# Performance work log

Measured on AMD Instinct MI355X. Metric: run time of the kernel, lower is better.

Reference implementation:

```python
import jax, jax.numpy as jnp
import numpy as np

INPUT_DIM = 64
HIDDEN_DIM = 128
N_ROWS = 2_000_000
N_GROUPS = 2


def setup_inputs() -> dict:
    key = jax.random.key(0)
    k_x, k_T, k_w1, k_b1, k_w2, k_b2 = jax.random.split(key, 6)
    x = jax.random.normal(k_x, (N_ROWS, INPUT_DIM), dtype=jnp.float32)
    T = jax.random.randint(k_T, (N_ROWS,), 0, N_GROUPS, dtype=jnp.int64)
    # Linear params (torch convention: W @ x layout -> y = x @ W.T + b)
    lim1 = 1.0 / np.sqrt(INPUT_DIM)
    W1 = jax.random.uniform(k_w1, (HIDDEN_DIM, INPUT_DIM), jnp.float32, -lim1, lim1)
    b1 = jax.random.uniform(k_b1, (HIDDEN_DIM,), jnp.float32, -lim1, lim1)
    lim2 = 1.0 / np.sqrt(HIDDEN_DIM)
    W2 = jax.random.uniform(k_w2, (1, HIDDEN_DIM), jnp.float32, -lim2, lim2)
    b2 = jax.random.uniform(k_b2, (1,), jnp.float32, -lim2, lim2)
    return {"x": x, "T": T, "W1": W1, "b1": b1, "W2": W2, "b2": b2}


def reference(x, T, W1, b1, W2, b2):
    # s = f2(tanh(f1(x))).flatten()  -> [N]
    h = jnp.tanh(x @ W1.T + b1)                      # [N, H]
    s = (h @ W2.T + b2).reshape(-1)                  # [N]
    e = jnp.exp(s)                                   # faithful to torch.exp (unshifted)
    # group sums via segment_sum (2 groups), then gather-normalize per row
    sums = jax.ops.segment_sum(e, T, num_segments=N_GROUPS)  # [2]
    return e / sums[T]
```

## Files before the change

### kernel.cpp

```cpp
#include <hip/hip_runtime.h>
#include <math.h>

#define NROWS 2000000
#define IN_DIM 64
#define HID 128
#define NTILES (NROWS / 16)

typedef __bf16 bf16x8 __attribute__((ext_vector_type(8)));
typedef float f32x4 __attribute__((ext_vector_type(4)));

__device__ __forceinline__ float tanh_fast(float a) {
    float p = __expf(2.0f * a);
    float r = __builtin_amdgcn_rcpf(p + 1.0f);
    return fmaf(-2.0f, r, 1.0f);
}

__device__ __forceinline__ void split8(f32x4 a, f32x4 b, bf16x8& h, bf16x8& l) {
    #pragma unroll
    for (int j = 0; j < 4; j++) {
        __bf16 hb = (__bf16)a[j];
        h[j] = hb;
        l[j] = (__bf16)(a[j] - (float)hb);
    }
    #pragma unroll
    for (int j = 0; j < 4; j++) {
        __bf16 hb = (__bf16)b[j];
        h[4 + j] = hb;
        l[4 + j] = (__bf16)(b[j] - (float)hb);
    }
}

__global__ void zero_sums_kernel(float* g) {
    if (threadIdx.x < 2) g[threadIdx.x] = 0.0f;
}

__global__ __launch_bounds__(256, 2) void fused_mfma_kernel(
    const float* __restrict__ x, const int* __restrict__ T,
    const float* __restrict__ W1, const float* __restrict__ b1,
    const float* __restrict__ W2, const float* __restrict__ b2,
    float* __restrict__ e_out, float* __restrict__ gsums)
{
    const int lane = threadIdx.x & 63;
    const int c16  = lane & 15;
    const int g4   = lane >> 4;
    const int gwave = blockIdx.x * (blockDim.x >> 6) + (threadIdx.x >> 6);
    const int nwave = gridDim.x * (blockDim.x >> 6);

    int tile = gwave;
    f32x4 xq0, xq1, xq2, xq3;
    {
        const float* xp = x + (size_t)(tile * 16 + c16) * IN_DIM + g4 * 8;
        xq0 = *(const f32x4*)(xp);
        xq1 = *(const f32x4*)(xp + 4);
        xq2 = *(const f32x4*)(xp + 32);
        xq3 = *(const f32x4*)(xp + 36);
    }

    bf16x8 w1h[8][2], w1l[8][2];
    #pragma unroll
    for (int t = 0; t < 8; t++) {
        #pragma unroll
        for (int c = 0; c < 2; c++) {
            const float* wp = W1 + (size_t)(t * 16 + c16) * IN_DIM + c * 32 + g4 * 8;
            f32x4 a = *(const f32x4*)wp;
            f32x4 b = *(const f32x4*)(wp + 4);
            split8(a, b, w1h[t][c], w1l[t][c]);
        }
    }
    float b1v[8], w2v[8];
    #pragma unroll
    for (int t = 0; t < 8; t++) {
        b1v[t] = b1[t * 16 + c16];
        w2v[t] = W2[t * 16 + c16];
    }
    const float b2v = b2[0];

    float ls0 = 0.f, ls1 = 0.f;

    for (; tile < NTILES; tile += nwave) {
        bf16x8 xh0, xh1, xl0, xl1;
        split8(xq0, xq1, xh0, xl0);
        split8(xq2, xq3, xh1, xl1);

        int nt = tile + nwave;
        if (nt < NTILES) {
            const float* xp = x + (size_t)(nt * 16 + c16) * IN_DIM + g4 * 8;
            xq0 = *(const f32x4*)(xp);
            xq1 = *(const f32x4*)(xp + 4);
            xq2 = *(const f32x4*)(xp + 32);
            xq3 = *(const f32x4*)(xp + 36);
        }

        f32x4 acc[8];
        #pragma unroll
        for (int t = 0; t < 8; t++) acc[t] = (f32x4){0.f, 0.f, 0.f, 0.f};
        #pragma unroll
        for (int t = 0; t < 8; t++) {
            acc[t] = __builtin_amdgcn_mfma_f32_16x16x32_bf16(xh0, w1h[t][0], acc[t], 0, 0, 0);
            acc[t] = __builtin_amdgcn_mfma_f32_16x16x32_bf16(xl0, w1h[t][0], acc[t], 0, 0, 0);
            acc[t] = __builtin_amdgcn_mfma_f32_16x16x32_bf16(xh0, w1l[t][0], acc[t], 0, 0, 0);
            acc[t] = __builtin_amdgcn_mfma_f32_16x16x32_bf16(xl0, w1l[t][0], acc[t], 0, 0, 0);
            acc[t] = __builtin_amdgcn_mfma_f32_16x16x32_bf16(xh1, w1h[t][1], acc[t], 0, 0, 0);
            acc[t] = __builtin_amdgcn_mfma_f32_16x16x32_bf16(xl1, w1h[t][1], acc[t], 0, 0, 0);
            acc[t] = __builtin_amdgcn_mfma_f32_16x16x32_bf16(xh1, w1l[t][1], acc[t], 0, 0, 0);
            acc[t] = __builtin_amdgcn_mfma_f32_16x16x32_bf16(xl1, w1l[t][1], acc[t], 0, 0, 0);
        }

        float sp0 = 0.f, sp1 = 0.f, sp2 = 0.f, sp3 = 0.f;
        #pragma unroll
        for (int t = 0; t < 8; t++) {
            sp0 = fmaf(tanh_fast(acc[t][0] + b1v[t]), w2v[t], sp0);
            sp1 = fmaf(tanh_fast(acc[t][1] + b1v[t]), w2v[t], sp1);
            sp2 = fmaf(tanh_fast(acc[t][2] + b1v[t]), w2v[t], sp2);
            sp3 = fmaf(tanh_fast(acc[t][3] + b1v[t]), w2v[t], sp3);
        }
        #pragma unroll
        for (int m = 1; m < 16; m <<= 1) {
            sp0 += __shfl_xor(sp0, m, 16);
            sp1 += __shfl_xor(sp1, m, 16);
            sp2 += __shfl_xor(sp2, m, 16);
            sp3 += __shfl_xor(sp3, m, 16);
        }
        if (c16 < 4) {
            float sv = (c16 == 0) ? sp0 : (c16 == 1) ? sp1 : (c16 == 2) ? sp2 : sp3;
            float e = __expf(sv + b2v);
            int row = tile * 16 + g4 * 4 + c16;
            e_out[row] = e;
            if (T[row] == 0) ls0 += e; else ls1 += e;
        }
    }

    #pragma unroll
    for (int off = 32; off > 0; off >>= 1) {
        ls0 += __shfl_down(ls0, off, 64);
        ls1 += __shfl_down(ls1, off, 64);
    }
    if (lane == 0) {
        atomicAdd(&gsums[0], ls0);
        atomicAdd(&gsums[1], ls1);
    }
}

__global__ __launch_bounds__(256) void normalize_kernel(
    float* __restrict__ e_out, const int* __restrict__ T,
    const float* __restrict__ gsums)
{
    const float inv0 = 1.0f / gsums[0];
    const float inv1 = 1.0f / gsums[1];
    const int n4 = NROWS / 4;
    const int stride = gridDim.x * blockDim.x;
    for (int i = blockIdx.x * blockDim.x + threadIdx.x; i < n4; i += stride) {
        float4 e = reinterpret_cast<const float4*>(e_out)[i];
        int4  t = reinterpret_cast<const int4*>(T)[i];
        e.x *= (t.x == 0) ? inv0 : inv1;
        e.y *= (t.y == 0) ? inv0 : inv1;
        e.z *= (t.z == 0) ? inv0 : inv1;
        e.w *= (t.w == 0) ? inv0 : inv1;
        reinterpret_cast<float4*>(e_out)[i] = e;
    }
}

extern "C" void kernel_launch(void* const* d_in, const int* in_sizes, int n_in,
                              void* d_out, int out_size, void* d_ws, size_t ws_size,
                              hipStream_t stream) {
    const float* x  = (const float*)d_in[0];
    const int*   T  = (const int*)d_in[1];
    const float* W1 = (const float*)d_in[2];
    const float* b1 = (const float*)d_in[3];
    const float* W2 = (const float*)d_in[4];
    const float* b2 = (const float*)d_in[5];
    float* e_out = (float*)d_out;
    float* gsums = (float*)d_ws;

    zero_sums_kernel<<<1, 64, 0, stream>>>(gsums);

    fused_mfma_kernel<<<512, 256, 0, stream>>>(x, T, W1, b1, W2, b2, e_out, gsums);

    normalize_kernel<<<2048, 256, 0, stream>>>(e_out, T, gsums);
}
```

Before: 199.1 us.

## Switch to single fp16 MFMA pass with LDS-staged weights and DPP reductions

```diff
diff --git a/kernel.cpp b/kernel.cpp
--- a/kernel.cpp
+++ b/kernel.cpp
@@ -5,8 +5,11 @@
 #define IN_DIM 64
 #define HID 128
 #define NTILES (NROWS / 16)
+#define BLOCK 256
+#define NBLK 1024
+#define WPB (BLOCK / 64)
 
-typedef __bf16 bf16x8 __attribute__((ext_vector_type(8)));
+typedef _Float16 half8 __attribute__((ext_vector_type(8)));
 typedef float f32x4 __attribute__((ext_vector_type(4)));
 
 __device__ __forceinline__ float tanh_fast(float a) {
@@ -15,58 +18,52 @@
     return fmaf(-2.0f, r, 1.0f);
 }
 
-__device__ __forceinline__ void split8(f32x4 a, f32x4 b, bf16x8& h, bf16x8& l) {
-    #pragma unroll
-    for (int j = 0; j < 4; j++) {
-        __bf16 hb = (__bf16)a[j];
-        h[j] = hb;
-        l[j] = (__bf16)(a[j] - (float)hb);
-    }
-    #pragma unroll
-    for (int j = 0; j < 4; j++) {
-        __bf16 hb = (__bf16)b[j];
-        h[4 + j] = hb;
-        l[4 + j] = (__bf16)(b[j] - (float)hb);
-    }
+__device__ __forceinline__ float dpp_row_sum16(float v) {
+    int x;
+    x = __float_as_int(v);
+    v += __int_as_float(__builtin_amdgcn_update_dpp(0, x, 0x111, 0xf, 0xf, true));
+    x = __float_as_int(v);
+    v += __int_as_float(__builtin_amdgcn_update_dpp(0, x, 0x112, 0xf, 0xf, true));
+    x = __float_as_int(v);
+    v += __int_as_float(__builtin_amdgcn_update_dpp(0, x, 0x114, 0xf, 0xf, true));
+    x = __float_as_int(v);
+    v += __int_as_float(__builtin_amdgcn_update_dpp(0, x, 0x118, 0xf, 0xf, true));
+    return v;
 }
 
 __global__ void zero_sums_kernel(float* g) {
     if (threadIdx.x < 2) g[threadIdx.x] = 0.0f;
 }
 
-__global__ __launch_bounds__(256, 2) void fused_mfma_kernel(
+__global__ __launch_bounds__(BLOCK, 4) void fused_mfma_kernel(
     const float* __restrict__ x, const int* __restrict__ T,
     const float* __restrict__ W1, const float* __restrict__ b1,
     const float* __restrict__ W2, const float* __restrict__ b2,
     float* __restrict__ e_out, float* __restrict__ gsums)
 {
+    __shared__ _Float16 wlds[8][2][64][8];
+
     const int lane = threadIdx.x & 63;
+    const int wv   = threadIdx.x >> 6;
     const int c16  = lane & 15;
     const int g4   = lane >> 4;
-    const int gwave = blockIdx.x * (blockDim.x >> 6) + (threadIdx.x >> 6);
-    const int nwave = gridDim.x * (blockDim.x >> 6);
 
-    int tile = gwave;
-    f32x4 xq0, xq1, xq2, xq3;
-    {
-        const float* xp = x + (size_t)(tile * 16 + c16) * IN_DIM + g4 * 8;
-        xq0 = *(const f32x4*)(xp);
-        xq1 = *(const f32x4*)(xp + 4);
-        xq2 = *(const f32x4*)(xp + 32);
-        xq3 = *(const f32x4*)(xp + 36);
-    }
-
-    bf16x8 w1h[8][2], w1l[8][2];
     #pragma unroll
-    for (int t = 0; t < 8; t++) {
+    for (int tt = 0; tt < 2; tt++) {
+        const int t = wv * 2 + tt;
+        const int n = t * 16 + c16;
         #pragma unroll
         for (int c = 0; c < 2; c++) {
-            const float* wp = W1 + (size_t)(t * 16 + c16) * IN_DIM + c * 32 + g4 * 8;
-            f32x4 a = *(const f32x4*)wp;
-            f32x4 b = *(const f32x4*)(wp + 4);
-            split8(a, b, w1h[t][c], w1l[t][c]);
+            const int kb = c * 32 + g4 * 8;
+            half8 h;
+            #pragma unroll
+            for (int j = 0; j < 8; j++)
+                h[j] = (_Float16)W1[n * IN_DIM + kb + j];
+            *(half8*)&wlds[t][c][lane][0] = h;
         }
     }
+    __syncthreads();
+
     float b1v[8], w2v[8];
     #pragma unroll
     for (int t = 0; t < 8; t++) {
@@ -75,20 +72,38 @@
     }
     const float b2v = b2[0];
 
+    const int gwave = blockIdx.x * WPB + wv;
+    const int nwave = NBLK * WPB;
+
     float ls0 = 0.f, ls1 = 0.f;
 
+    int tile = gwave;
+    f32x4 g0, g1, g2, g3;
+    {
+        const float* xp = x + (size_t)tile * 1024 + (size_t)c16 * IN_DIM + g4 * 8;
+        g0 = *(const f32x4*)(xp);
+        g1 = *(const f32x4*)(xp + 4);
+        g2 = *(const f32x4*)(xp + 32);
+        g3 = *(const f32x4*)(xp + 36);
+    }
+
     for (; tile < NTILES; tile += nwave) {
-        bf16x8 xh0, xh1, xl0, xl1;
-        split8(xq0, xq1, xh0, xl0);
-        split8(xq2, xq3, xh1, xl1);
+        half8 xf0, xf1;
+        #pragma unroll
+        for (int j = 0; j < 4; j++) {
+            xf0[j]     = (_Float16)g0[j];
+            xf0[4 + j] = (_Float16)g1[j];
+            xf1[j]     = (_Float16)g2[j];
+            xf1[4 + j] = (_Float16)g3[j];
+        }
 
-        int nt = tile + nwave;
+        const int nt = tile + nwave;
         if (nt < NTILES) {
-            const float* xp = x + (size_t)(nt * 16 + c16) * IN_DIM + g4 * 8;
-            xq0 = *(const f32x4*)(xp);
-            xq1 = *(const f32x4*)(xp + 4);
-            xq2 = *(const f32x4*)(xp + 32);
-            xq3 = *(const f32x4*)(xp + 36);
+            const float* xp = x + (size_t)nt * 1024 + (size_t)c16 * IN_DIM + g4 * 8;
+            g0 = *(const f32x4*)(xp);
+            g1 = *(const f32x4*)(xp + 4);
+            g2 = *(const f32x4*)(xp + 32);
+            g3 = *(const f32x4*)(xp + 36);
         }
 
         f32x4 acc[8];
@@ -96,14 +111,10 @@
         for (int t = 0; t < 8; t++) acc[t] = (f32x4){0.f, 0.f, 0.f, 0.f};
         #pragma unroll
         for (int t = 0; t < 8; t++) {
-            acc[t] = __builtin_amdgcn_mfma_f32_16x16x32_bf16(xh0, w1h[t][0], acc[t], 0, 0, 0);
-            acc[t] = __builtin_amdgcn_mfma_f32_16x16x32_bf16(xl0, w1h[t][0], acc[t], 0, 0, 0);
-            acc[t] = __builtin_amdgcn_mfma_f32_16x16x32_bf16(xh0, w1l[t][0], acc[t], 0, 0, 0);
-            acc[t] = __builtin_amdgcn_mfma_f32_16x16x32_bf16(xl0, w1l[t][0], acc[t], 0, 0, 0);
-            acc[t] = __builtin_amdgcn_mfma_f32_16x16x32_bf16(xh1, w1h[t][1], acc[t], 0, 0, 0);
-            acc[t] = __builtin_amdgcn_mfma_f32_16x16x32_bf16(xl1, w1h[t][1], acc[t], 0, 0, 0);
-            acc[t] = __builtin_amdgcn_mfma_f32_16x16x32_bf16(xh1, w1l[t][1], acc[t], 0, 0, 0);
-            acc[t] = __builtin_amdgcn_mfma_f32_16x16x32_bf16(xl1, w1l[t][1], acc[t], 0, 0, 0);
+            half8 w0 = *(const half8*)&wlds[t][0][lane][0];
+            half8 w1 = *(const half8*)&wlds[t][1][lane][0];
+            acc[t] = __builtin_amdgcn_mfma_f32_16x16x32_f16(xf0, w0, acc[t], 0, 0, 0);
+            acc[t] = __builtin_amdgcn_mfma_f32_16x16x32_f16(xf1, w1, acc[t], 0, 0, 0);
         }
 
         float sp0 = 0.f, sp1 = 0.f, sp2 = 0.f, sp3 = 0.f;
@@ -114,19 +125,23 @@
             sp2 = fmaf(tanh_fast(acc[t][2] + b1v[t]), w2v[t], sp2);
             sp3 = fmaf(tanh_fast(acc[t][3] + b1v[t]), w2v[t], sp3);
         }
-        #pragma unroll
-        for (int m = 1; m < 16; m <<= 1) {
-            sp0 += __shfl_xor(sp0, m, 16);
-            sp1 += __shfl_xor(sp1, m, 16);
-            sp2 += __shfl_xor(sp2, m, 16);
-            sp3 += __shfl_xor(sp3, m, 16);
-        }
-        if (c16 < 4) {
-            float sv = (c16 == 0) ? sp0 : (c16 == 1) ? sp1 : (c16 == 2) ? sp2 : sp3;
-            float e = __expf(sv + b2v);
-            int row = tile * 16 + g4 * 4 + c16;
-            e_out[row] = e;
-            if (T[row] == 0) ls0 += e; else ls1 += e;
+        sp0 = dpp_row_sum16(sp0);
+        sp1 = dpp_row_sum16(sp1);
+        sp2 = dpp_row_sum16(sp2);
+        sp3 = dpp_row_sum16(sp3);
+
+        if (c16 == 15) {
+            const int row0 = tile * 16 + g4 * 4;
+            float e0 = __expf(sp0 + b2v);
+            float e1 = __expf(sp1 + b2v);
+            float e2 = __expf(sp2 + b2v);
+            float e3 = __expf(sp3 + b2v);
+            *(f32x4*)&e_out[row0] = (f32x4){e0, e1, e2, e3};
+            int4 t4 = *(const int4*)&T[row0];
+            if (t4.x == 0) ls0 += e0; else ls1 += e0;
+            if (t4.y == 0) ls0 += e1; else ls1 += e1;
+            if (t4.z == 0) ls0 += e2; else ls1 += e2;
+            if (t4.w == 0) ls0 += e3; else ls1 += e3;
         }
     }
 
@@ -174,7 +189,7 @@
 
     zero_sums_kernel<<<1, 64, 0, stream>>>(gsums);
 
-    fused_mfma_kernel<<<512, 256, 0, stream>>>(x, T, W1, b1, W2, b2, e_out, gsums);
+    fused_mfma_kernel<<<NBLK, BLOCK, 0, stream>>>(x, T, W1, b1, W2, b2, e_out, gsums);
 
     normalize_kernel<<<2048, 256, 0, stream>>>(e_out, T, gsums);
 }
```

Result: slower. 254.6 us (+27.8%).
